# Performance work log

Hardware: AMD Instinct MI355X
Metric: run time of the kernel (lower is better)

The kernel has to match this reference:

```python
import jax, jax.numpy as jnp
import numpy as np
from jax import lax

# dims from init_kwargs: in_features=1920, out_features=1920, window_size=12
B = 1024
IN_F = 1920
OUT_F = 1920
WS = 12              # window_size (GRU input & hidden size)
K = IN_F // WS
OUT_WS = OUT_F // K  # per-block decoder output = 12
D_HID = 1024         # decoder hidden width


def sinusoidal_pe(L, d):
    # standard sinusoidal positional encoding, shape (L, d)
    pos = jnp.arange(L, dtype=jnp.float32)[:, None]
    div = jnp.exp(jnp.arange(0, d, 2, dtype=jnp.float32) * (-np.log(10000.0) / d))
    ang = pos * div  # (L, d//2)
    pe = jnp.zeros((L, d), jnp.float32)
    pe = pe.at[:, 0::2].set(jnp.sin(ang))
    pe = pe.at[:, 1::2].set(jnp.cos(ang))
    return pe


def gru(x, h0, Wih, Whh, bih, bhh):
    # x: (B, T, I) batch_first; PyTorch GRU gate order: r, z, n
    def step(h, xt):
        gi = xt @ Wih.T + bih          # (B, 3H)
        gh = h @ Whh.T + bhh           # (B, 3H)
        ir, iz, inn = jnp.split(gi, 3, axis=-1)
        hr, hz, hn = jnp.split(gh, 3, axis=-1)
        r = jax.nn.sigmoid(ir + hr)
        z = jax.nn.sigmoid(iz + hz)
        n = jnp.tanh(inn + r * hn)
        h_new = (1.0 - z) * n + z * h
        return h_new, h_new
    hT, ys = lax.scan(step, h0, jnp.swapaxes(x, 0, 1))
    return jnp.swapaxes(ys, 0, 1), hT


def setup_inputs() -> dict:
    key = jax.random.key(0)
    ks = jax.random.split(key, 11)
    s = lambda k, shape: jax.random.normal(k, shape, jnp.float32) * 0.05
    return {
        "x": jax.random.normal(ks[0], (B, IN_F), jnp.float32),
        # per-block segment encoders: Linear(WS, WS) x K
        "enc_W": s(ks[1], (K, WS, WS)),
        "enc_b": s(ks[2], (K, WS)),
        # shared GRU (input=hidden=WS)
        "Wih": s(ks[3], (3 * WS, WS)),
        "Whh": s(ks[4], (3 * WS, WS)),
        "bih": s(ks[5], (3 * WS,)),
        "bhh": s(ks[6], (3 * WS,)),
        # per-block decoders: Linear(WS,1024) -> Linear(1024,OUT_WS)
        "dec_W1": s(ks[7], (K, WS, D_HID)),
        "dec_b1": s(ks[8], (K, D_HID)),
        "dec_W2": s(ks[9], (K, D_HID, OUT_WS)),
        "dec_b2": s(ks[10], (K, OUT_WS)),
    }


def reference(x, enc_W, enc_b, Wih, Whh, bih, bhh, dec_W1, dec_b1, dec_W2, dec_b2):
    # SegmentationBlock: split (B, IN_F) -> (B, K, WS), per-block Linear+ReLU
    xb = x.reshape(B, K, WS)
    xs = jax.nn.relu(jnp.einsum('bki,kio->bko', xb, enc_W) + enc_b[None])

    # first GRU pass: only final hidden state h (B, WS)
    h0 = jnp.zeros((B, WS), x.dtype)
    _, h = gru(xs, h0, Wih, Whh, bih, bhh)

    # positional encodings (value-independent sinusoidal, broadcast over batch)
    pos_enc = sinusoidal_pe(K, WS)          # (K, WS)
    ch_pe = sinusoidal_pe(K, K)             # (K, K)
    # channel_enc[:, :, j] = channel_encs[:, :, j // K]  (fused gather)
    channel_enc = ch_pe[:, jnp.arange(WS) // K]  # (K, WS)

    x_enc = xs + pos_enc[None] + channel_enc[None]

    # second GRU pass initialized with h
    out, _ = gru(x_enc, h, Wih, Whh, bih, bhh)  # (B, K, WS)

    # per-block decoder MLPs (dropout is identity in eval)
    hid = jnp.einsum('bkd,kdh->bkh', out, dec_W1) + dec_b1[None]      # (B, K, 1024)
    res = jnp.einsum('bkh,kho->bko', hid, dec_W2) + dec_b2[None]      # (B, K, OUT_WS)
    return res.reshape(B, K * OUT_WS)[:, :OUT_F]
```

## Files before the change

kernel.cpp:

```cpp
#include <hip/hip_runtime.h>
#include <hip/hip_bf16.h>

using bf16 = __hip_bfloat16;

#define C1 1.44269504f
#define C2 2.88539008f

__device__ __forceinline__ float fexp2(float x) { return __builtin_amdgcn_exp2f(x); }
__device__ __forceinline__ float frcp(float x)  { return __builtin_amdgcn_rcpf(x); }
__device__ __forceinline__ float sigm2(float x) { return frcp(1.f + fexp2(-x)); }
__device__ __forceinline__ float tanh2(float x) { return 1.f - 2.f * frcp(1.f + fexp2(x)); }

__device__ __forceinline__ float bf2f(unsigned int u) {
    union { unsigned int u; float f; } c; c.u = u << 16; return c.f;
}
__device__ __forceinline__ unsigned int f2bfbits(float f) {
    union { float f; unsigned int u; } c; c.f = f;
    return (c.u + 0x7fffu + ((c.u >> 16) & 1u)) >> 16;
}

#define KSTR 12288
#define OFF_PEGI 15728640
#define OFF_WC   15759360

__global__ __launch_bounds__(256) void k_encode(
    const float* __restrict__ x, const float* __restrict__ encW, const float* __restrict__ encb,
    const float* __restrict__ Wih, const float* __restrict__ bih, const float* __restrict__ bhh,
    uint2* __restrict__ gi, float4* __restrict__ pegi)
{
    const int k = blockIdx.y, t = threadIdx.x;
    const int b = blockIdx.x * 256 + t;

    __shared__ float sW[144], sbm[12], sWih[432], sbih[36], spet[12];
    if (t < 144) sW[t]  = encW[k * 144 + t];
    if (t < 12)  sbm[t] = encb[k * 12 + t];
    for (int i = t; i < 432; i += 256) sWih[i] = Wih[i];
    if (t < 36)  sbih[t] = bih[t] + (t < 24 ? bhh[t] : 0.f);
    if (t < 12) {
        int m = t >> 1;
        float div = __expf((float)(2 * m) * (-0.7675283643313489f));
        float ang = (float)k * div;
        spet[t] = ((t & 1) ? cosf(ang) : sinf(ang)) + sinf((float)k);
    }
    __syncthreads();
    if (t < 12 && blockIdx.x == 0) {
        float sr = 0.f, sz = 0.f, sn = 0.f;
        #pragma unroll
        for (int o = 0; o < 12; o++) {
            sr = fmaf(spet[o], sWih[t * 12 + o], sr);
            sz = fmaf(spet[o], sWih[(12 + t) * 12 + o], sz);
            sn = fmaf(spet[o], sWih[(24 + t) * 12 + o], sn);
        }
        pegi[k * 12 + t] = make_float4(C1 * sr, C1 * sz, C2 * sn, 0.f);
    }

    const float4* xp = reinterpret_cast<const float4*>(x + (size_t)b * 1920 + k * 12);
    float4 a0 = xp[0], a1 = xp[1], a2 = xp[2];
    float xv[12] = {a0.x,a0.y,a0.z,a0.w, a1.x,a1.y,a1.z,a1.w, a2.x,a2.y,a2.z,a2.w};

    float xs[12];
    #pragma unroll
    for (int o = 0; o < 12; o++) {
        float s = sbm[o];
        #pragma unroll
        for (int i = 0; i < 12; i++) s = fmaf(xv[i], sW[i * 12 + o], s);
        xs[o] = fmaxf(s, 0.f);
    }

    uint2* g = gi + ((size_t)k * 1024 + b) * 12;
    #pragma unroll
    for (int j = 0; j < 12; j++) {
        float sr = sbih[j], sz = sbih[12 + j], sn = sbih[24 + j];
        #pragma unroll
        for (int o = 0; o < 12; o++) {
            sr = fmaf(xs[o], sWih[j * 12 + o], sr);
            sz = fmaf(xs[o], sWih[(12 + j) * 12 + o], sz);
            sn = fmaf(xs[o], sWih[(24 + j) * 12 + o], sn);
        }
        g[j] = make_uint2(f2bfbits(C1 * sr) | (f2bfbits(C1 * sz) << 16), f2bfbits(C2 * sn));
    }
}

__global__ __launch_bounds__(64) void k_recur(
    const float* __restrict__ Whh, const float* __restrict__ bhh,
    const uint2* __restrict__ gi, const float4* __restrict__ pegi,
    float* __restrict__ hout)
{
    const int lane = threadIdx.x;
    const int g = lane >> 4, j = lane & 15;
    const int ju = (j < 12) ? j : 0;
    const int b = blockIdx.x * 4 + g;
    const int src = lane & ~15;

    float wr[12], wz[12], wn[12];
    #pragma unroll
    for (int d = 0; d < 12; d++) {
        wr[d] = C1 * Whh[ju * 12 + d];
        wz[d] = C1 * Whh[(12 + ju) * 12 + d];
        wn[d] = C2 * Whh[(24 + ju) * 12 + d];
    }
    const float bn = C2 * bhh[24 + ju];

    const uint2* gp = gi + (size_t)b * 12 + ju;

    float h[12];
    #pragma unroll
    for (int d = 0; d < 12; d++) h[d] = 0.f;
    float hself = 0.f;

    uint2 buf[8];
    #pragma unroll
    for (int i = 0; i < 8; i++) buf[i] = gp[(size_t)i * KSTR];

    for (int ko = 0; ko < 160; ko += 8) {
        #pragma unroll
        for (int i = 0; i < 8; i++) {
            const int k = ko + i;
            float gr = bf2f(buf[i].x & 0xffffu);
            float gz = bf2f(buf[i].x >> 16);
            float gn = bf2f(buf[i].y & 0xffffu);
            int kp = k + 8; kp = (kp > 159) ? 159 : kp;
            buf[i] = gp[(size_t)kp * KSTR];
            float hr = 0.f, hz = 0.f, hn = bn;
            #pragma unroll
            for (int d = 0; d < 12; d++) {
                hr = fmaf(wr[d], h[d], hr);
                hz = fmaf(wz[d], h[d], hz);
                hn = fmaf(wn[d], h[d], hn);
            }
            float r = sigm2(gr + hr);
            float z = sigm2(gz + hz);
            float n = tanh2(fmaf(r, hn, gn));
            float hj = fmaf(z, hself - n, n);
            hself = hj;
            #pragma unroll
            for (int d = 0; d < 12; d++) h[d] = __shfl(hj, src + d, 64);
        }
    }

    float4 speb[8];
    #pragma unroll
    for (int i = 0; i < 8; i++) {
        buf[i]  = gp[(size_t)i * KSTR];
        speb[i] = pegi[i * 12 + ju];
    }
    float* ho = hout + (size_t)b * 1920;
    for (int ko = 0; ko < 160; ko += 8) {
        #pragma unroll
        for (int i = 0; i < 8; i++) {
            const int k = ko + i;
            float gr = bf2f(buf[i].x & 0xffffu) + speb[i].x;
            float gz = bf2f(buf[i].x >> 16)     + speb[i].y;
            float gn = bf2f(buf[i].y & 0xffffu) + speb[i].z;
            int kp = k + 8; kp = (kp > 159) ? 159 : kp;
            buf[i]  = gp[(size_t)kp * KSTR];
            speb[i] = pegi[kp * 12 + ju];
            float hr = 0.f, hz = 0.f, hn = bn;
            #pragma unroll
            for (int d = 0; d < 12; d++) {
                hr = fmaf(wr[d], h[d], hr);
                hz = fmaf(wz[d], h[d], hz);
                hn = fmaf(wn[d], h[d], hn);
            }
            float r = sigm2(gr + hr);
            float z = sigm2(gz + hz);
            float n = tanh2(fmaf(r, hn, gn));
            float hj = fmaf(z, hself - n, n);
            hself = hj;
            if (j < 12) ho[k * 12 + j] = hj;
            #pragma unroll
            for (int d = 0; d < 12; d++) h[d] = __shfl(hj, src + d, 64);
        }
    }
}

__global__ __launch_bounds__(256) void k_fold(
    const float* __restrict__ W1, const float* __restrict__ b1,
    const float* __restrict__ W2, const float* __restrict__ b2,
    float* __restrict__ Wcg)
{
    const int k = blockIdx.x, t = threadIdx.x;
    if (t >= 156) return;
    const int o = (t < 144) ? (t % 12) : (t - 144);
    const float* va = (t < 144) ? (W1 + (size_t)k * 12288 + (size_t)(t / 12) * 1024)
                                : (b1 + (size_t)k * 1024);
    const float* vb = W2 + (size_t)k * 12288 + o;
    const float4* va4 = reinterpret_cast<const float4*>(va);
    float s0 = 0.f, s1 = 0.f, s2 = 0.f, s3 = 0.f;
    #pragma unroll 4
    for (int q = 0; q < 256; q++) {
        float4 a = va4[q];
        const float* vbq = vb + q * 48;
        s0 = fmaf(a.x, vbq[0],  s0);
        s1 = fmaf(a.y, vbq[12], s1);
        s2 = fmaf(a.z, vbq[24], s2);
        s3 = fmaf(a.w, vbq[36], s3);
    }
    float s = (s0 + s1) + (s2 + s3);
    if (t >= 144) s += b2[k * 12 + o];
    Wcg[k * 156 + t] = s;
}

__global__ __launch_bounds__(256) void k_apply(
    const float* __restrict__ Wcg, float* __restrict__ out)
{
    const int k = blockIdx.x, t = threadIdx.x;
    __shared__ float sw[156];
    if (t < 156) sw[t] = Wcg[k * 156 + t];
    __syncthreads();

    for (int bb = t; bb < 1024; bb += 256) {
        float* hp = out + (size_t)bb * 1920 + k * 12;
        float4* h4 = reinterpret_cast<float4*>(hp);
        float4 a0 = h4[0], a1 = h4[1], a2 = h4[2];
        float hv[12] = {a0.x,a0.y,a0.z,a0.w, a1.x,a1.y,a1.z,a1.w, a2.x,a2.y,a2.z,a2.w};
        float ov[12];
        #pragma unroll
        for (int o = 0; o < 12; o++) {
            float s = sw[144 + o];
            #pragma unroll
            for (int d = 0; d < 12; d++) s = fmaf(hv[d], sw[d * 12 + o], s);
            ov[o] = s;
        }
        h4[0] = make_float4(ov[0], ov[1], ov[2],  ov[3]);
        h4[1] = make_float4(ov[4], ov[5], ov[6],  ov[7]);
        h4[2] = make_float4(ov[8], ov[9], ov[10], ov[11]);
    }
}

extern "C" void kernel_launch(void* const* d_in, const int* in_sizes, int n_in,
                              void* d_out, int out_size, void* d_ws, size_t ws_size,
                              hipStream_t stream)
{
    const float* x    = (const float*)d_in[0];
    const float* encW = (const float*)d_in[1];
    const float* encb = (const float*)d_in[2];
    const float* Wih  = (const float*)d_in[3];
    const float* Whh  = (const float*)d_in[4];
    const float* bih  = (const float*)d_in[5];
    const float* bhh  = (const float*)d_in[6];
    const float* W1   = (const float*)d_in[7];
    const float* b1   = (const float*)d_in[8];
    const float* W2   = (const float*)d_in[9];
    const float* b2   = (const float*)d_in[10];
    float* out = (float*)d_out;

    char* ws = (char*)d_ws;
    uint2*  gi   = (uint2*)(ws);
    float4* pegi = (float4*)(ws + OFF_PEGI);
    float*  Wcg  = (float*)(ws + OFF_WC);

    k_encode<<<dim3(4, 160), 256, 0, stream>>>(x, encW, encb, Wih, bih, bhh, gi, pegi);
    k_fold  <<<dim3(160),    256, 0, stream>>>(W1, b1, W2, b2, Wcg);
    k_recur <<<dim3(256),    64,  0, stream>>>(Whh, bhh, gi, pegi, out);
    k_apply <<<dim3(160),    256, 0, stream>>>(Wcg, out);
}
```

Before: 210.5 us.

## Interleave two batch chains per wave in GRU recurrence and stage encode/fold data in LDS

The recurrence kernel now runs two independent batch groups per wavefront, interleaving their GRU steps so one chain's latency is hidden by the other, and halves the grid to 128 blocks. It broadcasts hidden state with ds_bpermute, caches the positional gate bias in shared memory, and unpacks bf16 with cheaper bit ops. The encode kernel stages its gate outputs in shared memory so global stores are coalesced, and the fold kernel stages W2 and b1 in shared memory. Using fewer blocks leaves more of the GPU idle, and each thread needs more registers.

Result: slower. 280.7 us (+33.4%).

```diff
diff --git a/kernel.cpp b/kernel.cpp
--- a/kernel.cpp
+++ b/kernel.cpp
@@ -11,9 +11,6 @@
 __device__ __forceinline__ float sigm2(float x) { return frcp(1.f + fexp2(-x)); }
 __device__ __forceinline__ float tanh2(float x) { return 1.f - 2.f * frcp(1.f + fexp2(x)); }
 
-__device__ __forceinline__ float bf2f(unsigned int u) {
-    union { unsigned int u; float f; } c; c.u = u << 16; return c.f;
-}
 __device__ __forceinline__ unsigned int f2bfbits(float f) {
     union { float f; unsigned int u; } c; c.f = f;
     return (c.u + 0x7fffu + ((c.u >> 16) & 1u)) >> 16;
@@ -32,6 +29,7 @@
     const int b = blockIdx.x * 256 + t;
 
     __shared__ float sW[144], sbm[12], sWih[432], sbih[36], spet[12];
+    __shared__ uint2 st[256 * 13];
     if (t < 144) sW[t]  = encW[k * 144 + t];
     if (t < 12)  sbm[t] = encb[k * 12 + t];
     for (int i = t; i < 432; i += 256) sWih[i] = Wih[i];
@@ -67,7 +65,6 @@
         xs[o] = fmaxf(s, 0.f);
     }
 
-    uint2* g = gi + ((size_t)k * 1024 + b) * 12;
     #pragma unroll
     for (int j = 0; j < 12; j++) {
         float sr = sbih[j], sz = sbih[12 + j], sn = sbih[24 + j];
@@ -77,8 +74,40 @@
             sz = fmaf(xs[o], sWih[(12 + j) * 12 + o], sz);
             sn = fmaf(xs[o], sWih[(24 + j) * 12 + o], sn);
         }
-        g[j] = make_uint2(f2bfbits(C1 * sr) | (f2bfbits(C1 * sz) << 16), f2bfbits(C2 * sn));
-    }
+        st[t * 13 + j] = make_uint2(f2bfbits(C1 * sr) | (f2bfbits(C1 * sz) << 16),
+                                    f2bfbits(C2 * sn));
+    }
+    __syncthreads();
+    uint2* gbase = gi + (size_t)k * KSTR + (size_t)blockIdx.x * 3072;
+    for (int i = t; i < 3072; i += 256) {
+        int bl = i / 12;
+        gbase[i] = st[bl * 13 + (i - bl * 12)];
+    }
+}
+
+__device__ __forceinline__ float gru_gates(float gr, float gz, float gn,
+                                           const float* wr, const float* wz, const float* wn,
+                                           float bn, const float* h, float hself)
+{
+    float hr = 0.f, hz = 0.f, hn = bn;
+    #pragma unroll
+    for (int d = 0; d < 12; d++) {
+        hr = fmaf(wr[d], h[d], hr);
+        hz = fmaf(wz[d], h[d], hz);
+        hn = fmaf(wn[d], h[d], hn);
+    }
+    float r = sigm2(gr + hr);
+    float z = sigm2(gz + hz);
+    float n = tanh2(fmaf(r, hn, gn));
+    return fmaf(z, hself - n, n);
+}
+
+__device__ __forceinline__ void bcast12(float* h, float hj, const int* ba)
+{
+    int v = __float_as_int(hj);
+    #pragma unroll
+    for (int d = 0; d < 12; d++)
+        h[d] = __int_as_float(__builtin_amdgcn_ds_bpermute(ba[d], v));
 }
 
 __global__ __launch_bounds__(64) void k_recur(
@@ -86,11 +115,18 @@
     const uint2* __restrict__ gi, const float4* __restrict__ pegi,
     float* __restrict__ hout)
 {
+    __shared__ float4 spe[1920];
     const int lane = threadIdx.x;
+    for (int i = lane; i < 1920; i += 64) spe[i] = pegi[i];
+
     const int g = lane >> 4, j = lane & 15;
     const int ju = (j < 12) ? j : 0;
-    const int b = blockIdx.x * 4 + g;
-    const int src = lane & ~15;
+    const int bA = blockIdx.x * 8 + g;
+    const int bB = bA + 4;
+
+    int ba[12];
+    #pragma unroll
+    for (int d = 0; d < 12; d++) ba[d] = ((lane & ~15) + d) << 2;
 
     float wr[12], wz[12], wn[12];
     #pragma unroll
@@ -100,76 +136,73 @@
         wn[d] = C2 * Whh[(24 + ju) * 12 + d];
     }
     const float bn = C2 * bhh[24 + ju];
-
-    const uint2* gp = gi + (size_t)b * 12 + ju;
-
-    float h[12];
-    #pragma unroll
-    for (int d = 0; d < 12; d++) h[d] = 0.f;
-    float hself = 0.f;
-
-    uint2 buf[8];
-    #pragma unroll
-    for (int i = 0; i < 8; i++) buf[i] = gp[(size_t)i * KSTR];
-
-    for (int ko = 0; ko < 160; ko += 8) {
-        #pragma unroll
-        for (int i = 0; i < 8; i++) {
+    __syncthreads();
+
+    const uint2* gpA = gi + (size_t)bA * 12 + ju;
+    const uint2* gpB = gi + (size_t)bB * 12 + ju;
+
+    float hA[12], hB[12], hsA = 0.f, hsB = 0.f;
+    #pragma unroll
+    for (int d = 0; d < 12; d++) { hA[d] = 0.f; hB[d] = 0.f; }
+
+    uint2 bufA[4], bufB[4];
+    #pragma unroll
+    for (int i = 0; i < 4; i++) { bufA[i] = gpA[(size_t)i * KSTR]; bufB[i] = gpB[(size_t)i * KSTR]; }
+
+    for (int ko = 0; ko < 160; ko += 4) {
+        #pragma unroll
+        for (int i = 0; i < 4; i++) {
             const int k = ko + i;
-            float gr = bf2f(buf[i].x & 0xffffu);
-            float gz = bf2f(buf[i].x >> 16);
-            float gn = bf2f(buf[i].y & 0xffffu);
-            int kp = k + 8; kp = (kp > 159) ? 159 : kp;
-            buf[i] = gp[(size_t)kp * KSTR];
-            float hr = 0.f, hz = 0.f, hn = bn;
-            #pragma unroll
-            for (int d = 0; d < 12; d++) {
-                hr = fmaf(wr[d], h[d], hr);
-                hz = fmaf(wz[d], h[d], hz);
-                hn = fmaf(wn[d], h[d], hn);
-            }
-            float r = sigm2(gr + hr);
-            float z = sigm2(gz + hz);
-            float n = tanh2(fmaf(r, hn, gn));
-            float hj = fmaf(z, hself - n, n);
-            hself = hj;
-            #pragma unroll
-            for (int d = 0; d < 12; d++) h[d] = __shfl(hj, src + d, 64);
-        }
-    }
-
-    float4 speb[8];
-    #pragma unroll
-    for (int i = 0; i < 8; i++) {
-        buf[i]  = gp[(size_t)i * KSTR];
-        speb[i] = pegi[i * 12 + ju];
-    }
-    float* ho = hout + (size_t)b * 1920;
-    for (int ko = 0; ko < 160; ko += 8) {
-        #pragma unroll
-        for (int i = 0; i < 8; i++) {
+            const int kp = (k + 4 > 159) ? 159 : k + 4;
+            float grA = __int_as_float((int)(bufA[i].x << 16));
+            float gzA = __int_as_float((int)(bufA[i].x & 0xffff0000u));
+            float gnA = __int_as_float((int)(bufA[i].y << 16));
+            bufA[i] = gpA[(size_t)kp * KSTR];
+            float hjA = gru_gates(grA, gzA, gnA, wr, wz, wn, bn, hA, hsA);
+            hsA = hjA;
+            bcast12(hA, hjA, ba);
+            float grB = __int_as_float((int)(bufB[i].x << 16));
+            float gzB = __int_as_float((int)(bufB[i].x & 0xffff0000u));
+            float gnB = __int_as_float((int)(bufB[i].y << 16));
+            bufB[i] = gpB[(size_t)kp * KSTR];
+            float hjB = gru_gates(grB, gzB, gnB, wr, wz, wn, bn, hB, hsB);
+            hsB = hjB;
+            bcast12(hB, hjB, ba);
+        }
+    }
+
+    float4 spb[4];
+    #pragma unroll
+    for (int i = 0; i < 4; i++) {
+        bufA[i] = gpA[(size_t)i * KSTR];
+        bufB[i] = gpB[(size_t)i * KSTR];
+        spb[i]  = spe[i * 12 + ju];
+    }
+    float* hoA = hout + (size_t)bA * 1920;
+    float* hoB = hout + (size_t)bB * 1920;
+    for (int ko = 0; ko < 160; ko += 4) {
+        #pragma unroll
+        for (int i = 0; i < 4; i++) {
             const int k = ko + i;
-            float gr = bf2f(buf[i].x & 0xffffu) + speb[i].x;
-            float gz = bf2f(buf[i].x >> 16)     + speb[i].y;
-            float gn = bf2f(buf[i].y & 0xffffu) + speb[i].z;
-            int kp = k + 8; kp = (kp > 159) ? 159 : kp;
-            buf[i]  = gp[(size_t)kp * KSTR];
-            speb[i] = pegi[kp * 12 + ju];
-            float hr = 0.f, hz = 0.f, hn = bn;
-            #pragma unroll
-            for (int d = 0; d < 12; d++) {
-                hr = fmaf(wr[d], h[d], hr);
-                hz = fmaf(wz[d], h[d], hz);
-                hn = fmaf(wn[d], h[d], hn);
-            }
-            float r = sigm2(gr + hr);
-            float z = sigm2(gz + hz);
-            float n = tanh2(fmaf(r, hn, gn));
-            float hj = fmaf(z, hself - n, n);
-            hself = hj;
-            if (j < 12) ho[k * 12 + j] = hj;
-            #pragma unroll
-            for (int d = 0; d < 12; d++) h[d] = __shfl(hj, src + d, 64);
+            const int kp = (k + 4 > 159) ? 159 : k + 4;
+            float4 sp = spb[i];
+            spb[i] = spe[kp * 12 + ju];
+            float grA = __int_as_float((int)(bufA[i].x << 16))        + sp.x;
+            float gzA = __int_as_float((int)(bufA[i].x & 0xffff0000u)) + sp.y;
+            float gnA = __int_as_float((int)(bufA[i].y << 16))        + sp.z;
+            bufA[i] = gpA[(size_t)kp * KSTR];
+            float hjA = gru_gates(grA, gzA, gnA, wr, wz, wn, bn, hA, hsA);
+            hsA = hjA;
+            if (j < 12) hoA[k * 12 + j] = hjA;
+            bcast12(hA, hjA, ba);
+            float grB = __int_as_float((int)(bufB[i].x << 16))        + sp.x;
+            float gzB = __int_as_float((int)(bufB[i].x & 0xffff0000u)) + sp.y;
+            float gnB = __int_as_float((int)(bufB[i].y << 16))        + sp.z;
+            bufB[i] = gpB[(size_t)kp * KSTR];
+            float hjB = gru_gates(grB, gzB, gnB, wr, wz, wn, bn, hB, hsB);
+            hsB = hjB;
+            if (j < 12) hoB[k * 12 + j] = hjB;
+            bcast12(hB, hjB, ba);
         }
     }
 }
@@ -180,21 +213,40 @@
     float* __restrict__ Wcg)
 {
     const int k = blockIdx.x, t = threadIdx.x;
+    __shared__ float sB[12288];
+    __shared__ float sb1[1024];
+    {
+        const float4* w2p = reinterpret_cast<const float4*>(W2 + (size_t)k * 12288);
+        float4* sB4 = reinterpret_cast<float4*>(sB);
+        for (int i = t; i < 3072; i += 256) sB4[i] = w2p[i];
+        const float4* b1p = reinterpret_cast<const float4*>(b1 + (size_t)k * 1024);
+        float4* sb14 = reinterpret_cast<float4*>(sb1);
+        if (t < 256) sb14[t] = b1p[t];
+    }
+    __syncthreads();
     if (t >= 156) return;
     const int o = (t < 144) ? (t % 12) : (t - 144);
-    const float* va = (t < 144) ? (W1 + (size_t)k * 12288 + (size_t)(t / 12) * 1024)
-                                : (b1 + (size_t)k * 1024);
-    const float* vb = W2 + (size_t)k * 12288 + o;
-    const float4* va4 = reinterpret_cast<const float4*>(va);
     float s0 = 0.f, s1 = 0.f, s2 = 0.f, s3 = 0.f;
-    #pragma unroll 4
-    for (int q = 0; q < 256; q++) {
-        float4 a = va4[q];
-        const float* vbq = vb + q * 48;
-        s0 = fmaf(a.x, vbq[0],  s0);
-        s1 = fmaf(a.y, vbq[12], s1);
-        s2 = fmaf(a.z, vbq[24], s2);
-        s3 = fmaf(a.w, vbq[36], s3);
+    if (t < 144) {
+        const float4* va4 = reinterpret_cast<const float4*>(W1 + (size_t)k * 12288 + (size_t)(t / 12) * 1024);
+        #pragma unroll 4
+        for (int q = 0; q < 256; q++) {
+            float4 a = va4[q];
+            const float* bq = sB + q * 48 + o;
+            s0 = fmaf(a.x, bq[0],  s0);
+            s1 = fmaf(a.y, bq[12], s1);
+            s2 = fmaf(a.z, bq[24], s2);
+            s3 = fmaf(a.w, bq[36], s3);
+        }
+    } else {
+        #pragma unroll 4
+        for (int hh = 0; hh < 1024; hh += 4) {
+            const float* bq = sB + hh * 12 + o;
+            s0 = fmaf(sb1[hh],     bq[0],  s0);
+            s1 = fmaf(sb1[hh + 1], bq[12], s1);
+            s2 = fmaf(sb1[hh + 2], bq[24], s2);
+            s3 = fmaf(sb1[hh + 3], bq[36], s3);
+        }
     }
     float s = (s0 + s1) + (s2 + s3);
     if (t >= 144) s += b2[k * 12 + o];
@@ -252,6 +304,6 @@
 
     k_encode<<<dim3(4, 160), 256, 0, stream>>>(x, encW, encb, Wih, bih, bhh, gi, pegi);
     k_fold  <<<dim3(160),    256, 0, stream>>>(W1, b1, W2, b2, Wcg);
-    k_recur <<<dim3(256),    64,  0, stream>>>(Whh, bhh, gi, pegi, out);
+    k_recur <<<dim3(128),    64,  0, stream>>>(Whh, bhh, gi, pegi, out);
     k_apply <<<dim3(160),    256, 0, stream>>>(Wcg, out);
 }
```
